# Optimization experiments

Hardware: AMD Instinct MI355X
Metric: run time of the kernel (lower is better)

Reference implementation:

```python
import jax, jax.numpy as jnp
import numpy as np

EPS = 1e-5

def _conv1x1(x, w, b):
    # x: (b,c,h,w), w: (o,c) -> (b,o,h,w)
    return jnp.einsum('bchw,oc->bohw', x, w) + b[None, :, None, None]

def _maxpool2(x):
    b, c, h, w = x.shape
    return x.reshape(b, c, h // 2, 2, w // 2, 2).max(axis=(3, 5))

def setup_inputs() -> dict:
    key = jax.random.key(0)
    ks = jax.random.split(key, 11)
    C, CI, H, W, B = 256, 128, 64, 64, 8
    s = 0.05
    return {
        'x': jax.random.normal(ks[0], (B, C, H, W), jnp.float32),
        'Wg': jax.random.normal(ks[1], (CI, C), jnp.float32) * s,
        'bg': jax.random.normal(ks[2], (CI,), jnp.float32) * s,
        'Wt': jax.random.normal(ks[3], (CI, C), jnp.float32) * s,
        'bt': jax.random.normal(ks[4], (CI,), jnp.float32) * s,
        'Wp': jax.random.normal(ks[5], (CI, C), jnp.float32) * s,
        'bp': jax.random.normal(ks[6], (CI,), jnp.float32) * s,
        'Ww': jax.random.normal(ks[7], (C, CI), jnp.float32) * s,
        'bw': jax.random.normal(ks[8], (C,), jnp.float32) * s,
        'gamma': jax.random.normal(ks[9], (C,), jnp.float32),
        'beta': jax.random.normal(ks[10], (C,), jnp.float32),
    }

def reference(x, Wg, bg, Wt, bt, Wp, bp, Ww, bw, gamma, beta):
    b, C, H, W = x.shape
    CI = Wg.shape[0]
    # g and phi are sub-sampled by 2x2 max pool -> M = (H/2)*(W/2); theta keeps N = H*W
    g_x = _maxpool2(_conv1x1(x, Wg, bg)).reshape(b, CI, -1).transpose(0, 2, 1)   # (b,M,ci)
    theta_x = _conv1x1(x, Wt, bt).reshape(b, CI, -1).transpose(0, 2, 1)          # (b,N,ci)
    phi_x = _maxpool2(_conv1x1(x, Wp, bp)).reshape(b, CI, -1)                    # (b,ci,M)
    f = jnp.einsum('bnc,bcm->bnm', theta_x, phi_x)                               # (b,N,M)
    f_div_C = jax.nn.softmax(f, axis=-1)
    y = jnp.einsum('bnm,bmc->bnc', f_div_C, g_x)                                 # (b,N,ci)
    y = y.transpose(0, 2, 1).reshape(b, CI, H, W)
    # W: 1x1 conv + BatchNorm2d (training mode: batch statistics, biased var)
    wy = _conv1x1(y, Ww, bw)
    mean = wy.mean(axis=(0, 2, 3), keepdims=True)
    var = ((wy - mean) ** 2).mean(axis=(0, 2, 3), keepdims=True)
    wy = (wy - mean) * jax.lax.rsqrt(var + EPS)
    wy = wy * gamma[None, :, None, None] + beta[None, :, None, None]
    z = wy + x
    # self.avg_pool is AdaptiveMaxPool2d(1): global spatial max
    return z.max(axis=(2, 3), keepdims=True)
```

## Files before the change

### kernel.cpp

```cpp
#include <hip/hip_runtime.h>
#include <hip/hip_bf16.h>
#include <stdint.h>

using f32x4  = __attribute__((ext_vector_type(4))) float;
using bf16x8 = __attribute__((ext_vector_type(8))) short;
using short4v = __attribute__((ext_vector_type(4))) short;

#define DEVINL static __device__ __forceinline__

DEVINL short f2bf(float f) {
    union { float f; uint32_t u; } v; v.f = f;
    uint32_t r = (v.u + 0x7FFFu + ((v.u >> 16) & 1u)) >> 16;
    return (short)(uint16_t)r;
}
DEVINL float bf2f(short s) {
    union { uint32_t u; float f; } v; v.u = ((uint32_t)(uint16_t)s) << 16;
    return v.f;
}
DEVINL float fexp2(float x) {
    float r;
    asm("v_exp_f32 %0, %1" : "=v"(r) : "v"(x));
    return r;
}
DEVINL uint32_t pk2bf(float a, float b) {
    union { __hip_bfloat162 v; uint32_t u; } c;
    c.v = __float22bfloat162_rn(float2{a, b});
    return c.u;
}

DEVINL void gld16(const short* g, short* l) {
    __builtin_amdgcn_global_load_lds(
        (const __attribute__((address_space(1))) unsigned int*)g,
        (__attribute__((address_space(3))) unsigned int*)l, 16, 0, 0);
}

#define LOG2E 1.44269504f

__global__ __launch_bounds__(256) void k0_prep(
        const float* __restrict__ Wg, const float* __restrict__ Wt, const float* __restrict__ Wp,
        const float* __restrict__ bg, const float* __restrict__ bt, const float* __restrict__ bp,
        const float* __restrict__ Ww,
        short* __restrict__ W_all, short* __restrict__ Ww16, float* __restrict__ b_all) {
    int i = blockIdx.x * 256 + threadIdx.x;
    if (i < 384 * 256) {
        int r = i >> 8, c = i & 255;
        float v = (r < 128) ? Wg[r * 256 + c]
                : (r < 256) ? Wt[(r - 128) * 256 + c] * LOG2E
                            : Wp[(r - 256) * 256 + c];
        W_all[i] = f2bf(v);
    } else if (i < 384 * 256 + 256 * 128) {
        int j = i - 384 * 256;
        Ww16[j] = f2bf(Ww[j]);
    }
    if (i < 384) {
        b_all[i] = (i < 128) ? bg[i] : (i < 256) ? bt[i - 128] * LOG2E : bp[i - 256];
    }
}

__global__ __launch_bounds__(256) void k1_conv(const float* __restrict__ x,
        const short* __restrict__ W_all, const float* __restrict__ b_all,
        short* __restrict__ OutT, short* __restrict__ Kmat, short* __restrict__ Vmat) {
    __shared__ short xs[128 * 32];
    __shared__ short obuf[128 * 128];
    const int ntile = blockIdx.x;
    const int otile = blockIdx.y;
    const int b     = blockIdx.z;
    const int tid  = threadIdx.x;
    const int lane = tid & 63;
    const int wave = tid >> 6;
    const int wn = wave >> 1, wo = wave & 1;
    const int l15 = lane & 15, lh = lane >> 4;

    f32x4 acc[4][4];
    #pragma unroll
    for (int i = 0; i < 4; i++)
        #pragma unroll
        for (int j = 0; j < 4; j++) acc[i][j] = f32x4{0.f, 0.f, 0.f, 0.f};

    const int n0 = ntile * 128;
    const int ob = otile * 128 + wo * 64;
    const float* xb = x + (size_t)b * 256 * 4096;

    const int srow_base = (lane & 15) + wave * 16;
    const int sc0 = (lane >> 4) * 8;

    for (int kt = 0; kt < 8; kt++) {
        __syncthreads();
        #pragma unroll
        for (int p = 0; p < 2; p++) {
            int row = srow_base + p * 64;
            const float* xp = xb + (size_t)(kt * 32 + sc0) * 4096 + n0 + row;
            bf16x8 w8;
            #pragma unroll
            for (int j = 0; j < 8; j++) w8[j] = f2bf(xp[(size_t)j * 4096]);
            int ch = (sc0 >> 3) ^ ((row >> 1) & 3);
            *(bf16x8*)&xs[row * 32 + ch * 8] = w8;
        }
        __syncthreads();

        bf16x8 a[4], w[4];
        #pragma unroll
        for (int nf = 0; nf < 4; nf++) {
            int row = wn * 64 + nf * 16 + l15;
            int ch  = lh ^ ((row >> 1) & 3);
            a[nf] = *(const bf16x8*)&xs[row * 32 + ch * 8];
        }
        #pragma unroll
        for (int of = 0; of < 4; of++)
            w[of] = *(const bf16x8*)(W_all + (size_t)(ob + of * 16 + l15) * 256 + kt * 32 + lh * 8);
        #pragma unroll
        for (int nf = 0; nf < 4; nf++)
            #pragma unroll
            for (int of = 0; of < 4; of++)
                acc[nf][of] = __builtin_amdgcn_mfma_f32_16x16x32_bf16(a[nf], w[of], acc[nf][of], 0, 0, 0);
    }

    #pragma unroll
    for (int of = 0; of < 4; of++) {
        int ocol = wo * 64 + of * 16 + l15;
        float bias = b_all[otile * 128 + ocol];
        #pragma unroll
        for (int nf = 0; nf < 4; nf++)
            #pragma unroll
            for (int r = 0; r < 4; r++) {
                int n  = wn * 64 + nf * 16 + lh * 4 + r;
                int ch = (ocol >> 3) ^ (n & 15);
                obuf[n * 128 + ch * 8 + (ocol & 7)] = f2bf(acc[nf][of][r] + bias);
            }
    }
    __syncthreads();

    if (otile == 1) {
        #pragma unroll
        for (int p = 0; p < 8; p++) {
            int n  = wave * 4 + lh + p * 16;
            int ch = l15 ^ (n & 15);
            bf16x8 v = *(const bf16x8*)&obuf[n * 128 + ch * 8];
            *(bf16x8*)(OutT + ((size_t)b * 4096 + n0 + n) * 128 + l15 * 8) = v;
        }
    } else if (otile == 2) {
        const int wp = tid >> 3;
        const int cc = (tid & 7) * 16;
        short* kdst = Kmat + ((size_t)b * 1024 + ntile * 32 + wp) * 128 + cc;
        #pragma unroll
        for (int cblk = 0; cblk < 2; cblk++) {
            const int chunk = (cc >> 3) + cblk;
            float mx[8];
            #pragma unroll
            for (int j = 0; j < 8; j++) mx[j] = -1e30f;
            #pragma unroll
            for (int q4 = 0; q4 < 4; q4++) {
                int n = (q4 >> 1) * 64 + 2 * wp + (q4 & 1);
                bf16x8 v = *(const bf16x8*)&obuf[n * 128 + ((chunk ^ (n & 15)) * 8)];
                #pragma unroll
                for (int j = 0; j < 8; j++) mx[j] = fmaxf(mx[j], bf2f(v[j]));
            }
            bf16x8 vo;
            #pragma unroll
            for (int j = 0; j < 8; j++) vo[j] = f2bf(mx[j]);
            *(bf16x8*)(kdst + cblk * 8) = vo;
        }
    } else {
        const int c   = tid >> 1;
        const int wp0 = (tid & 1) * 16;
        const int chb = c >> 3, cl = c & 7;
        #pragma unroll
        for (int half = 0; half < 2; half++) {
            bf16x8 vo;
            #pragma unroll
            for (int j = 0; j < 8; j++) {
                int wp = wp0 + half * 8 + j;
                float mx = -1e30f;
                #pragma unroll
                for (int q4 = 0; q4 < 4; q4++) {
                    int n = (q4 >> 1) * 64 + 2 * wp + (q4 & 1);
                    mx = fmaxf(mx, bf2f(obuf[n * 128 + ((chb ^ (n & 15)) * 8) + cl]));
                }
                vo[j] = f2bf(mx);
            }
            *(bf16x8*)(Vmat + ((size_t)b * 128 + c) * 1024 + ntile * 32 + wp0 + half * 8) = vo;
        }
    }
}

__global__ __launch_bounds__(256) void k3_attn(const short* __restrict__ OutT,
        const short* __restrict__ Kmat, const short* __restrict__ Vmat,
        const short* __restrict__ Ww16, const float* __restrict__ bw,
        short* __restrict__ wy) {
    __shared__ short smem[36864];
    short* const sKb = smem;
    short* const sVb = smem + 16384;
    short* const sPb = smem + 32768;

    const int bid = blockIdx.x;
    const int b   = bid & 7;
    const int nt  = bid >> 3;
    const int tid = threadIdx.x;
    const int lane = tid & 63;
    const int wave = tid >> 6;
    const int l15 = lane & 15, lh = lane >> 4;
    const int nblk = nt * 64;
    const int n0 = nblk + wave * 16;

    const short* Kb = Kmat + (size_t)b * 1024 * 128;
    const short* Vb = Vmat + (size_t)b * 128 * 1024;
    short* sPw = sPb + wave * 1024;

    auto STAGE = [&](int t, int bufi) {
        const int m0 = t * 64;
        #pragma unroll
        for (int i = 0; i < 4; i++) {
            const int segb = (i * 4 + wave) * 64;
            const int rowK = (segb >> 4) + (lane >> 4);
            const int chkK = lane & 15;
            gld16(Kb + (size_t)(m0 + rowK) * 128 + ((chkK ^ (rowK & 15)) << 3),
                  sKb + bufi * 8192 + segb * 8);
            const int rowV = (segb >> 3) + (lane >> 3);
            const int chkV = lane & 7;
            gld16(Vb + (size_t)rowV * 1024 + m0 + ((chkV ^ (rowV & 7)) << 3),
                  sVb + bufi * 8192 + segb * 8);
        }
    };

    bf16x8 q[4];
    {
        const short* qrow = OutT + ((size_t)b * 4096 + n0 + l15) * 128;
        #pragma unroll
        for (int ks = 0; ks < 4; ks++)
            q[ks] = *(const bf16x8*)(qrow + ks * 32 + lh * 8);
    }

    f32x4 y[8];
    #pragma unroll
    for (int cf = 0; cf < 8; cf++) y[cf] = f32x4{0.f, 0.f, 0.f, 0.f};
    float mrun = -1e30f, lrun = 0.f;

    STAGE(0, 0);
    int cur = 0;

    for (int t = 0; t < 16; t++) {
        if (t < 15) {
            STAGE(t + 1, cur ^ 1);
            asm volatile("s_waitcnt vmcnt(8)" ::: "memory");
        } else {
            asm volatile("s_waitcnt vmcnt(0)" ::: "memory");
        }
        __builtin_amdgcn_s_barrier();
        __builtin_amdgcn_sched_barrier(0);

        const short* cK = sKb + cur * 8192;
        const short* cV = sVb + cur * 8192;

        f32x4 S[4];
        #pragma unroll
        for (int mf = 0; mf < 4; mf++) S[mf] = f32x4{0.f, 0.f, 0.f, 0.f};
        #pragma unroll
        for (int ks = 0; ks < 4; ks++) {
            bf16x8 kf[4];
            #pragma unroll
            for (int mf = 0; mf < 4; mf++) {
                int mrow = mf * 16 + l15;
                int jj   = ks * 4 + lh;
                kf[mf] = *(const bf16x8*)&cK[mrow * 128 + ((jj ^ (mrow & 15)) << 3)];
            }
            __builtin_amdgcn_s_setprio(1);
            #pragma unroll
            for (int mf = 0; mf < 4; mf++)
                S[mf] = __builtin_amdgcn_mfma_f32_16x16x32_bf16(kf[mf], q[ks], S[mf], 0, 0, 0);
            __builtin_amdgcn_s_setprio(0);
        }

        float pm = S[0][0];
        #pragma unroll
        for (int mf = 0; mf < 4; mf++)
            #pragma unroll
            for (int r = 0; r < 4; r++) pm = fmaxf(pm, S[mf][r]);
        pm = fmaxf(pm, __shfl_xor(pm, 16));
        pm = fmaxf(pm, __shfl_xor(pm, 32));

        if (__any(pm > mrun + 8.656f)) {
            float mnew  = fmaxf(mrun, pm);
            float alpha = fexp2(mrun - mnew);
            mrun = mnew;
            lrun *= alpha;
            float aR[4];
            #pragma unroll
            for (int r = 0; r < 4; r++) aR[r] = __shfl(alpha, lh * 4 + r);
            #pragma unroll
            for (int cf = 0; cf < 8; cf++)
                #pragma unroll
                for (int r = 0; r < 4; r++) y[cf][r] *= aR[r];
        }
        float rs = 0.f;
        #pragma unroll
        for (int mf = 0; mf < 4; mf++)
            #pragma unroll
            for (int r = 0; r < 4; r++) {
                float p = fexp2(S[mf][r] - mrun);
                S[mf][r] = p;
                rs += p;
            }
        rs += __shfl_xor(rs, 16);
        rs += __shfl_xor(rs, 32);
        lrun += rs;

        #pragma unroll
        for (int mf = 0; mf < 4; mf++) {
            uint2 pk = { pk2bf(S[mf][0], S[mf][1]), pk2bf(S[mf][2], S[mf][3]) };
            *(uint2*)&sPw[(l15 << 6) + (((mf * 4 + lh) ^ l15) << 2)] = pk;
        }

        #pragma unroll
        for (int ks2 = 0; ks2 < 2; ks2++) {
            int u0 = ks2 * 8 + lh * 2;
            short4v lo = *(const short4v*)&sPw[(l15 << 6) + (((u0)     ^ l15) << 2)];
            short4v hi = *(const short4v*)&sPw[(l15 << 6) + (((u0 + 1) ^ l15) << 2)];
            bf16x8 pa = { lo.x, lo.y, lo.z, lo.w, hi.x, hi.y, hi.z, hi.w };
            int jj = ks2 * 4 + lh;
            __builtin_amdgcn_s_setprio(1);
            #pragma unroll
            for (int cf = 0; cf < 8; cf++) {
                int crow = cf * 16 + l15;
                bf16x8 vf = *(const bf16x8*)&cV[crow * 64 + ((jj ^ (crow & 7)) << 3)];
                y[cf] = __builtin_amdgcn_mfma_f32_16x16x32_bf16(pa, vf, y[cf], 0, 0, 0);
            }
            __builtin_amdgcn_s_setprio(0);
        }

        __builtin_amdgcn_sched_barrier(0);
        __builtin_amdgcn_s_barrier();
        cur ^= 1;
    }

    float linv[4];
    #pragma unroll
    for (int r = 0; r < 4; r++) linv[r] = 1.f / __shfl(lrun, lh * 4 + r);

    short* const Yt = smem;
    #pragma unroll
    for (int cf = 0; cf < 8; cf++) {
        int c = cf * 16 + l15;
        #pragma unroll
        for (int r = 0; r < 4; r++) {
            int n = wave * 16 + lh * 4 + r;
            Yt[n * 128 + (((c >> 3) ^ (n & 15)) << 3) + (c & 7)] = f2bf(y[cf][r] * linv[r]);
        }
    }
    __syncthreads();

    bf16x8 by[4][4];
    #pragma unroll
    for (int nf = 0; nf < 4; nf++)
        #pragma unroll
        for (int ks = 0; ks < 4; ks++) {
            int n  = nf * 16 + l15;
            int kc = ks * 4 + lh;
            by[nf][ks] = *(const bf16x8*)&Yt[n * 128 + ((kc ^ (n & 15)) << 3)];
        }

    short* const sOut = smem + 8192 + wave * 4608;
    const int obase = wave * 64;
    #pragma unroll
    for (int of = 0; of < 4; of++) {
        bf16x8 aw[4];
        #pragma unroll
        for (int ks = 0; ks < 4; ks++)
            aw[ks] = *(const bf16x8*)(Ww16 + (size_t)(obase + of * 16 + l15) * 128 + ks * 32 + lh * 8);
        #pragma unroll
        for (int nf = 0; nf < 4; nf++) {
            f32x4 acc = f32x4{0.f, 0.f, 0.f, 0.f};
            #pragma unroll
            for (int ks = 0; ks < 4; ks++)
                acc = __builtin_amdgcn_mfma_f32_16x16x32_bf16(aw[ks], by[nf][ks], acc, 0, 0, 0);
            #pragma unroll
            for (int r = 0; r < 4; r++) {
                int o_loc = of * 16 + lh * 4 + r;
                sOut[o_loc * 72 + nf * 16 + l15] = f2bf(acc[r] + bw[obase + o_loc]);
            }
        }
    }

    #pragma unroll
    for (int p = 0; p < 8; p++) {
        int o_loc = p * 8 + (lane >> 3);
        int n8    = (lane & 7) * 8;
        bf16x8 v = *(const bf16x8*)&sOut[o_loc * 72 + n8];
        *(bf16x8*)(wy + ((size_t)b * 256 + obase + o_loc) * 4096 + nblk + n8) = v;
    }
}

__global__ __launch_bounds__(512) void k45_bnmax(const short* __restrict__ wy,
        const float* __restrict__ x,
        const float* __restrict__ gamma, const float* __restrict__ beta,
        float* __restrict__ outp) {
    const int o   = blockIdx.x;
    const int tid = threadIdx.x;
    const int lane = tid & 63;
    const int wave = tid >> 6;

    bf16x8 w8[8];
    float s = 0.f, s2 = 0.f;
    #pragma unroll
    for (int b = 0; b < 8; b++) {
        w8[b] = *(const bf16x8*)(wy + ((size_t)b * 256 + o) * 4096 + tid * 8);
        #pragma unroll
        for (int j = 0; j < 8; j++) {
            float f = bf2f(w8[b][j]);
            s += f; s2 += f * f;
        }
    }
    #pragma unroll
    for (int off = 1; off < 64; off <<= 1) { s += __shfl_xor(s, off); s2 += __shfl_xor(s2, off); }
    __shared__ float sred[8][2];
    if (lane == 0) { sred[wave][0] = s; sred[wave][1] = s2; }
    __syncthreads();
    s = 0.f; s2 = 0.f;
    #pragma unroll
    for (int wv = 0; wv < 8; wv++) { s += sred[wv][0]; s2 += sred[wv][1]; }
    float mean = s * (1.f / 32768.f);
    float var  = s2 * (1.f / 32768.f) - mean * mean;
    float rstd = rsqrtf(var + 1e-5f);
    float A = rstd * gamma[o];
    float B = beta[o] - mean * A;

    float mx[8];
    #pragma unroll
    for (int b = 0; b < 8; b++) {
        const float* px = x + ((size_t)b * 256 + o) * 4096 + tid * 8;
        float4 xa = *(const float4*)px;
        float4 xb = *(const float4*)(px + 4);
        float m = bf2f(w8[b][0]) * A + B + xa.x;
        m = fmaxf(m, bf2f(w8[b][1]) * A + B + xa.y);
        m = fmaxf(m, bf2f(w8[b][2]) * A + B + xa.z);
        m = fmaxf(m, bf2f(w8[b][3]) * A + B + xa.w);
        m = fmaxf(m, bf2f(w8[b][4]) * A + B + xb.x);
        m = fmaxf(m, bf2f(w8[b][5]) * A + B + xb.y);
        m = fmaxf(m, bf2f(w8[b][6]) * A + B + xb.z);
        m = fmaxf(m, bf2f(w8[b][7]) * A + B + xb.w);
        mx[b] = m;
    }
    #pragma unroll
    for (int b = 0; b < 8; b++)
        #pragma unroll
        for (int off = 1; off < 64; off <<= 1) mx[b] = fmaxf(mx[b], __shfl_xor(mx[b], off));
    __shared__ float mred[8][8];
    if (lane == 0) {
        #pragma unroll
        for (int b = 0; b < 8; b++) mred[wave][b] = mx[b];
    }
    __syncthreads();
    if (tid < 8) {
        float m = mred[0][tid];
        #pragma unroll
        for (int wv = 1; wv < 8; wv++) m = fmaxf(m, mred[wv][tid]);
        outp[tid * 256 + o] = m;
    }
}

extern "C" void kernel_launch(void* const* d_in, const int* in_sizes, int n_in,
                              void* d_out, int out_size, void* d_ws, size_t ws_size,
                              hipStream_t stream) {
    const float* x     = (const float*)d_in[0];
    const float* Wg    = (const float*)d_in[1];
    const float* bg    = (const float*)d_in[2];
    const float* Wt    = (const float*)d_in[3];
    const float* bt    = (const float*)d_in[4];
    const float* Wp    = (const float*)d_in[5];
    const float* bp    = (const float*)d_in[6];
    const float* Ww    = (const float*)d_in[7];
    const float* bw    = (const float*)d_in[8];
    const float* gamma = (const float*)d_in[9];
    const float* beta  = (const float*)d_in[10];
    float* outp = (float*)d_out;

    char* ws = (char*)d_ws;
    size_t off = 0;
    auto alloc = [&](size_t bytes) -> void* {
        void* p = ws + off;
        off = (off + bytes + 255) & ~(size_t)255;
        return p;
    };
    short* W_all = (short*)alloc((size_t)384 * 256 * 2);
    short* Ww16  = (short*)alloc((size_t)256 * 128 * 2);
    float* b_all = (float*)alloc((size_t)384 * 4);
    short* OutT  = (short*)alloc((size_t)8 * 4096 * 128 * 2);
    short* Kmat  = (short*)alloc((size_t)8 * 1024 * 128 * 2);
    short* Vmat  = (short*)alloc((size_t)8 * 128 * 1024 * 2);
    short* wy    = (short*)alloc((size_t)8 * 256 * 4096 * 2);

    k0_prep<<<512, 256, 0, stream>>>(Wg, Wt, Wp, bg, bt, bp, Ww, W_all, Ww16, b_all);
    k1_conv<<<dim3(32, 3, 8), 256, 0, stream>>>(x, W_all, b_all, OutT, Kmat, Vmat);
    k3_attn<<<512, 256, 0, stream>>>(OutT, Kmat, Vmat, Ww16, bw, wy);
    k45_bnmax<<<256, 512, 0, stream>>>(wy, x, gamma, beta, outp);
}
```

Measured before the change: 86.25 us.

## Switch attention kernel to 32x32x16 MFMA tiles with two waves per block

The attention kernel now uses 32x32x16 bf16 MFMA instructions instead of 16x16x32 and runs two waves per block, each owning 32 query rows. The softmax reductions, P staging layout, output projection and staging loops are remapped to the 32x32 accumulator layout. The aim is better MFMA throughput and fewer LDS fragment reads per FLOP. In exchange each wave holds more accumulator registers and there are fewer waves per block, which can lower latency hiding.

```diff
diff --git a/kernel.cpp b/kernel.cpp
--- a/kernel.cpp
+++ b/kernel.cpp
@@ -3,6 +3,7 @@
 #include <stdint.h>
 
 using f32x4  = __attribute__((ext_vector_type(4))) float;
+using f32x16 = __attribute__((ext_vector_type(16))) float;
 using bf16x8 = __attribute__((ext_vector_type(8))) short;
 using short4v = __attribute__((ext_vector_type(4))) short;
 
@@ -183,11 +184,11 @@
     }
 }
 
-__global__ __launch_bounds__(256) void k3_attn(const short* __restrict__ OutT,
+__global__ __launch_bounds__(128) void k3_attn(const short* __restrict__ OutT,
         const short* __restrict__ Kmat, const short* __restrict__ Vmat,
         const short* __restrict__ Ww16, const float* __restrict__ bw,
         short* __restrict__ wy) {
-    __shared__ short smem[36864];
+    __shared__ short smem[34816];
     short* const sKb = smem;
     short* const sVb = smem + 16384;
     short* const sPb = smem + 32768;
@@ -198,19 +199,19 @@
     const int tid = threadIdx.x;
     const int lane = tid & 63;
     const int wave = tid >> 6;
-    const int l15 = lane & 15, lh = lane >> 4;
+    const int l31 = lane & 31, hi = lane >> 5;
     const int nblk = nt * 64;
-    const int n0 = nblk + wave * 16;
+    const int n0 = nblk + wave * 32;
 
     const short* Kb = Kmat + (size_t)b * 1024 * 128;
     const short* Vb = Vmat + (size_t)b * 128 * 1024;
-    short* sPw = sPb + wave * 1024;
+    short* const sPw = sPb + wave * 1024;
 
     auto STAGE = [&](int t, int bufi) {
         const int m0 = t * 64;
         #pragma unroll
-        for (int i = 0; i < 4; i++) {
-            const int segb = (i * 4 + wave) * 64;
+        for (int i = 0; i < 8; i++) {
+            const int segb = (i * 2 + wave) * 64;
             const int rowK = (segb >> 4) + (lane >> 4);
             const int chkK = lane & 15;
             gld16(Kb + (size_t)(m0 + rowK) * 128 + ((chkK ^ (rowK & 15)) << 3),
@@ -222,17 +223,19 @@
         }
     };
 
-    bf16x8 q[4];
+    bf16x8 qf[8];
     {
-        const short* qrow = OutT + ((size_t)b * 4096 + n0 + l15) * 128;
-        #pragma unroll
-        for (int ks = 0; ks < 4; ks++)
-            q[ks] = *(const bf16x8*)(qrow + ks * 32 + lh * 8);
-    }
-
-    f32x4 y[8];
-    #pragma unroll
-    for (int cf = 0; cf < 8; cf++) y[cf] = f32x4{0.f, 0.f, 0.f, 0.f};
+        const short* qrow = OutT + ((size_t)b * 4096 + n0 + l31) * 128;
+        #pragma unroll
+        for (int step = 0; step < 8; step++)
+            qf[step] = *(const bf16x8*)(qrow + step * 16 + hi * 8);
+    }
+
+    f32x16 y[4];
+    #pragma unroll
+    for (int ct = 0; ct < 4; ct++)
+        #pragma unroll
+        for (int e = 0; e < 16; e++) y[ct][e] = 0.f;
     float mrun = -1e30f, lrun = 0.f;
 
     STAGE(0, 0);
@@ -241,7 +244,7 @@
     for (int t = 0; t < 16; t++) {
         if (t < 15) {
             STAGE(t + 1, cur ^ 1);
-            asm volatile("s_waitcnt vmcnt(8)" ::: "memory");
+            asm volatile("s_waitcnt vmcnt(16)" ::: "memory");
         } else {
             asm volatile("s_waitcnt vmcnt(0)" ::: "memory");
         }
@@ -251,31 +254,32 @@
         const short* cK = sKb + cur * 8192;
         const short* cV = sVb + cur * 8192;
 
-        f32x4 S[4];
-        #pragma unroll
-        for (int mf = 0; mf < 4; mf++) S[mf] = f32x4{0.f, 0.f, 0.f, 0.f};
-        #pragma unroll
-        for (int ks = 0; ks < 4; ks++) {
-            bf16x8 kf[4];
-            #pragma unroll
-            for (int mf = 0; mf < 4; mf++) {
-                int mrow = mf * 16 + l15;
-                int jj   = ks * 4 + lh;
-                kf[mf] = *(const bf16x8*)&cK[mrow * 128 + ((jj ^ (mrow & 15)) << 3)];
+        f32x16 S[2];
+        #pragma unroll
+        for (int mt = 0; mt < 2; mt++)
+            #pragma unroll
+            for (int e = 0; e < 16; e++) S[mt][e] = 0.f;
+        #pragma unroll
+        for (int step = 0; step < 8; step++) {
+            bf16x8 kf[2];
+            #pragma unroll
+            for (int mt = 0; mt < 2; mt++) {
+                int mrow = mt * 32 + l31;
+                int chk  = step * 2 + hi;
+                kf[mt] = *(const bf16x8*)&cK[mrow * 128 + ((chk ^ (mrow & 15)) << 3)];
             }
             __builtin_amdgcn_s_setprio(1);
             #pragma unroll
-            for (int mf = 0; mf < 4; mf++)
-                S[mf] = __builtin_amdgcn_mfma_f32_16x16x32_bf16(kf[mf], q[ks], S[mf], 0, 0, 0);
+            for (int mt = 0; mt < 2; mt++)
+                S[mt] = __builtin_amdgcn_mfma_f32_32x32x16_bf16(kf[mt], qf[step], S[mt], 0, 0, 0);
             __builtin_amdgcn_s_setprio(0);
         }
 
         float pm = S[0][0];
         #pragma unroll
-        for (int mf = 0; mf < 4; mf++)
-            #pragma unroll
-            for (int r = 0; r < 4; r++) pm = fmaxf(pm, S[mf][r]);
-        pm = fmaxf(pm, __shfl_xor(pm, 16));
+        for (int mt = 0; mt < 2; mt++)
+            #pragma unroll
+            for (int e = 0; e < 16; e++) pm = fmaxf(pm, S[mt][e]);
         pm = fmaxf(pm, __shfl_xor(pm, 32));
 
         if (__any(pm > mrun + 8.656f)) {
@@ -283,48 +287,52 @@
             float alpha = fexp2(mrun - mnew);
             mrun = mnew;
             lrun *= alpha;
-            float aR[4];
-            #pragma unroll
-            for (int r = 0; r < 4; r++) aR[r] = __shfl(alpha, lh * 4 + r);
-            #pragma unroll
-            for (int cf = 0; cf < 8; cf++)
+            float aR[16];
+            #pragma unroll
+            for (int r = 0; r < 16; r++)
+                aR[r] = __shfl(alpha, (r & 3) + 8 * (r >> 2) + 4 * hi);
+            #pragma unroll
+            for (int ct = 0; ct < 4; ct++)
                 #pragma unroll
-                for (int r = 0; r < 4; r++) y[cf][r] *= aR[r];
+                for (int r = 0; r < 16; r++) y[ct][r] *= aR[r];
         }
         float rs = 0.f;
         #pragma unroll
-        for (int mf = 0; mf < 4; mf++)
-            #pragma unroll
-            for (int r = 0; r < 4; r++) {
-                float p = fexp2(S[mf][r] - mrun);
-                S[mf][r] = p;
+        for (int mt = 0; mt < 2; mt++)
+            #pragma unroll
+            for (int e = 0; e < 16; e++) {
+                float p = fexp2(S[mt][e] - mrun);
+                S[mt][e] = p;
                 rs += p;
             }
-        rs += __shfl_xor(rs, 16);
         rs += __shfl_xor(rs, 32);
         lrun += rs;
 
         #pragma unroll
-        for (int mf = 0; mf < 4; mf++) {
-            uint2 pk = { pk2bf(S[mf][0], S[mf][1]), pk2bf(S[mf][2], S[mf][3]) };
-            *(uint2*)&sPw[(l15 << 6) + (((mf * 4 + lh) ^ l15) << 2)] = pk;
-        }
-
-        #pragma unroll
-        for (int ks2 = 0; ks2 < 2; ks2++) {
-            int u0 = ks2 * 8 + lh * 2;
-            short4v lo = *(const short4v*)&sPw[(l15 << 6) + (((u0)     ^ l15) << 2)];
-            short4v hi = *(const short4v*)&sPw[(l15 << 6) + (((u0 + 1) ^ l15) << 2)];
-            bf16x8 pa = { lo.x, lo.y, lo.z, lo.w, hi.x, hi.y, hi.z, hi.w };
-            int jj = ks2 * 4 + lh;
-            __builtin_amdgcn_s_setprio(1);
-            #pragma unroll
-            for (int cf = 0; cf < 8; cf++) {
-                int crow = cf * 16 + l15;
-                bf16x8 vf = *(const bf16x8*)&cV[crow * 64 + ((jj ^ (crow & 7)) << 3)];
-                y[cf] = __builtin_amdgcn_mfma_f32_16x16x32_bf16(pa, vf, y[cf], 0, 0, 0);
-            }
-            __builtin_amdgcn_s_setprio(0);
+        for (int mt = 0; mt < 2; mt++) {
+            #pragma unroll
+            for (int g = 0; g < 4; g++) {
+                uint2 pk = { pk2bf(S[mt][g * 4 + 0], S[mt][g * 4 + 1]),
+                             pk2bf(S[mt][g * 4 + 2], S[mt][g * 4 + 3]) };
+                int mb4 = 2 * g + hi;
+                *(uint2*)&sPw[(l31 << 5) + ((mb4 ^ (l31 & 7)) << 2)] = pk;
+            }
+            #pragma unroll
+            for (int ks = 0; ks < 2; ks++) {
+                int c0 = ks * 4 + 2 * hi;
+                short4v lo = *(const short4v*)&sPw[(l31 << 5) + (((c0)     ^ (l31 & 7)) << 2)];
+                short4v h4 = *(const short4v*)&sPw[(l31 << 5) + (((c0 + 1) ^ (l31 & 7)) << 2)];
+                bf16x8 pa = { lo.x, lo.y, lo.z, lo.w, h4.x, h4.y, h4.z, h4.w };
+                __builtin_amdgcn_s_setprio(1);
+                #pragma unroll
+                for (int ct = 0; ct < 4; ct++) {
+                    int c   = ct * 32 + l31;
+                    int chk = mt * 4 + ks * 2 + hi;
+                    bf16x8 vf = *(const bf16x8*)&cV[c * 64 + ((chk ^ (c & 7)) << 3)];
+                    y[ct] = __builtin_amdgcn_mfma_f32_32x32x16_bf16(pa, vf, y[ct], 0, 0, 0);
+                }
+                __builtin_amdgcn_s_setprio(0);
+            }
         }
 
         __builtin_amdgcn_sched_barrier(0);
@@ -332,56 +340,54 @@
         cur ^= 1;
     }
 
-    float linv[4];
-    #pragma unroll
-    for (int r = 0; r < 4; r++) linv[r] = 1.f / __shfl(lrun, lh * 4 + r);
-
+    float linv[16];
+    #pragma unroll
+    for (int r = 0; r < 16; r++)
+        linv[r] = 1.f / __shfl(lrun, (r & 3) + 8 * (r >> 2) + 4 * hi);
+
+    __syncthreads();
     short* const Yt = smem;
     #pragma unroll
-    for (int cf = 0; cf < 8; cf++) {
-        int c = cf * 16 + l15;
-        #pragma unroll
-        for (int r = 0; r < 4; r++) {
-            int n = wave * 16 + lh * 4 + r;
-            Yt[n * 128 + (((c >> 3) ^ (n & 15)) << 3) + (c & 7)] = f2bf(y[cf][r] * linv[r]);
+    for (int ct = 0; ct < 4; ct++) {
+        int c = ct * 32 + l31;
+        #pragma unroll
+        for (int r = 0; r < 16; r++) {
+            int n = wave * 32 + (r & 3) + 8 * (r >> 2) + 4 * hi;
+            Yt[n * 128 + (((c >> 3) ^ (n & 15)) << 3) + (c & 7)] = f2bf(y[ct][r] * linv[r]);
         }
     }
     __syncthreads();
 
-    bf16x8 by[4][4];
-    #pragma unroll
-    for (int nf = 0; nf < 4; nf++)
-        #pragma unroll
-        for (int ks = 0; ks < 4; ks++) {
-            int n  = nf * 16 + l15;
-            int kc = ks * 4 + lh;
-            by[nf][ks] = *(const bf16x8*)&Yt[n * 128 + ((kc ^ (n & 15)) << 3)];
-        }
-
-    short* const sOut = smem + 8192 + wave * 4608;
-    const int obase = wave * 64;
-    #pragma unroll
-    for (int of = 0; of < 4; of++) {
-        bf16x8 aw[4];
-        #pragma unroll
-        for (int ks = 0; ks < 4; ks++)
-            aw[ks] = *(const bf16x8*)(Ww16 + (size_t)(obase + of * 16 + l15) * 128 + ks * 32 + lh * 8);
-        #pragma unroll
-        for (int nf = 0; nf < 4; nf++) {
-            f32x4 acc = f32x4{0.f, 0.f, 0.f, 0.f};
-            #pragma unroll
-            for (int ks = 0; ks < 4; ks++)
-                acc = __builtin_amdgcn_mfma_f32_16x16x32_bf16(aw[ks], by[nf][ks], acc, 0, 0, 0);
-            #pragma unroll
-            for (int r = 0; r < 4; r++) {
-                int o_loc = of * 16 + lh * 4 + r;
-                sOut[o_loc * 72 + nf * 16 + l15] = f2bf(acc[r] + bw[obase + o_loc]);
-            }
-        }
-    }
-
-    #pragma unroll
-    for (int p = 0; p < 8; p++) {
+    short* const sOut = smem + 8192 + wave * 9216;
+    const int obase = wave * 128;
+    #pragma unroll
+    for (int ot = 0; ot < 4; ot++) {
+        bf16x8 aw[8];
+        #pragma unroll
+        for (int step = 0; step < 8; step++)
+            aw[step] = *(const bf16x8*)(Ww16 + (size_t)(obase + ot * 32 + l31) * 128 + step * 16 + hi * 8);
+        #pragma unroll
+        for (int nt2 = 0; nt2 < 2; nt2++) {
+            f32x16 acc;
+            #pragma unroll
+            for (int e = 0; e < 16; e++) acc[e] = 0.f;
+            #pragma unroll
+            for (int step = 0; step < 8; step++) {
+                int n   = nt2 * 32 + l31;
+                int chk = step * 2 + hi;
+                bf16x8 byf = *(const bf16x8*)&Yt[n * 128 + ((chk ^ (n & 15)) << 3)];
+                acc = __builtin_amdgcn_mfma_f32_32x32x16_bf16(aw[step], byf, acc, 0, 0, 0);
+            }
+            #pragma unroll
+            for (int r = 0; r < 16; r++) {
+                int o_loc = ot * 32 + (r & 3) + 8 * (r >> 2) + 4 * hi;
+                sOut[o_loc * 72 + nt2 * 32 + l31] = f2bf(acc[r] + bw[obase + o_loc]);
+            }
+        }
+    }
+
+    #pragma unroll
+    for (int p = 0; p < 16; p++) {
         int o_loc = p * 8 + (lane >> 3);
         int n8    = (lane & 7) * 8;
         bf16x8 v = *(const bf16x8*)&sOut[o_loc * 72 + n8];
@@ -490,6 +496,6 @@
 
     k0_prep<<<512, 256, 0, stream>>>(Wg, Wt, Wp, bg, bt, bp, Ww, W_all, Ww16, b_all);
     k1_conv<<<dim3(32, 3, 8), 256, 0, stream>>>(x, W_all, b_all, OutT, Kmat, Vmat);
-    k3_attn<<<512, 256, 0, stream>>>(OutT, Kmat, Vmat, Ww16, bw, wy);
+    k3_attn<<<512, 128, 0, stream>>>(OutT, Kmat, Vmat, Ww16, bw, wy);
     k45_bnmax<<<256, 512, 0, stream>>>(wy, x, gamma, beta, outp);
 }
```

New measurement: 95.63 us. +10.9%, slower.

## Compute all three 1x1 conv projections per block to reuse loaded x tile

Applied to the files above, without the earlier changes.

The conv kernel now handles all three projection output tiles (g, theta, phi) in a single block instead of launching a separate block per output tile. Each x tile is loaded from global memory and converted to bf16 once instead of three times, cutting global reads of the input. In exchange, each block holds three times as many accumulators, raising register pressure. The grid also shrinks to 256 blocks, which may reduce occupancy and latency hiding.

```diff
diff --git a/kernel.cpp b/kernel.cpp
--- a/kernel.cpp
+++ b/kernel.cpp
@@ -63,22 +63,22 @@
     __shared__ short xs[128 * 32];
     __shared__ short obuf[128 * 128];
     const int ntile = blockIdx.x;
-    const int otile = blockIdx.y;
-    const int b     = blockIdx.z;
+    const int b     = blockIdx.y;
     const int tid  = threadIdx.x;
     const int lane = tid & 63;
     const int wave = tid >> 6;
     const int wn = wave >> 1, wo = wave & 1;
     const int l15 = lane & 15, lh = lane >> 4;
 
-    f32x4 acc[4][4];
-    #pragma unroll
-    for (int i = 0; i < 4; i++)
-        #pragma unroll
-        for (int j = 0; j < 4; j++) acc[i][j] = f32x4{0.f, 0.f, 0.f, 0.f};
+    f32x4 acc[3][4][4];
+    #pragma unroll
+    for (int ot = 0; ot < 3; ot++)
+        #pragma unroll
+        for (int i = 0; i < 4; i++)
+            #pragma unroll
+            for (int j = 0; j < 4; j++) acc[ot][i][j] = f32x4{0.f, 0.f, 0.f, 0.f};
 
     const int n0 = ntile * 128;
-    const int ob = otile * 128 + wo * 64;
     const float* xb = x + (size_t)b * 256 * 4096;
 
     const int srow_base = (lane & 15) + wave * 16;
@@ -98,7 +98,7 @@
         }
         __syncthreads();
 
-        bf16x8 a[4], w[4];
+        bf16x8 a[4];
         #pragma unroll
         for (int nf = 0; nf < 4; nf++) {
             int row = wn * 64 + nf * 16 + l15;
@@ -106,79 +106,87 @@
             a[nf] = *(const bf16x8*)&xs[row * 32 + ch * 8];
         }
         #pragma unroll
-        for (int of = 0; of < 4; of++)
-            w[of] = *(const bf16x8*)(W_all + (size_t)(ob + of * 16 + l15) * 256 + kt * 32 + lh * 8);
-        #pragma unroll
-        for (int nf = 0; nf < 4; nf++)
+        for (int ot = 0; ot < 3; ot++) {
+            bf16x8 w[4];
             #pragma unroll
             for (int of = 0; of < 4; of++)
-                acc[nf][of] = __builtin_amdgcn_mfma_f32_16x16x32_bf16(a[nf], w[of], acc[nf][of], 0, 0, 0);
-    }
-
-    #pragma unroll
-    for (int of = 0; of < 4; of++) {
-        int ocol = wo * 64 + of * 16 + l15;
-        float bias = b_all[otile * 128 + ocol];
-        #pragma unroll
-        for (int nf = 0; nf < 4; nf++)
-            #pragma unroll
-            for (int r = 0; r < 4; r++) {
-                int n  = wn * 64 + nf * 16 + lh * 4 + r;
-                int ch = (ocol >> 3) ^ (n & 15);
-                obuf[n * 128 + ch * 8 + (ocol & 7)] = f2bf(acc[nf][of][r] + bias);
-            }
-    }
-    __syncthreads();
-
-    if (otile == 1) {
-        #pragma unroll
-        for (int p = 0; p < 8; p++) {
-            int n  = wave * 4 + lh + p * 16;
-            int ch = l15 ^ (n & 15);
-            bf16x8 v = *(const bf16x8*)&obuf[n * 128 + ch * 8];
-            *(bf16x8*)(OutT + ((size_t)b * 4096 + n0 + n) * 128 + l15 * 8) = v;
-        }
-    } else if (otile == 2) {
-        const int wp = tid >> 3;
-        const int cc = (tid & 7) * 16;
-        short* kdst = Kmat + ((size_t)b * 1024 + ntile * 32 + wp) * 128 + cc;
-        #pragma unroll
-        for (int cblk = 0; cblk < 2; cblk++) {
-            const int chunk = (cc >> 3) + cblk;
-            float mx[8];
-            #pragma unroll
-            for (int j = 0; j < 8; j++) mx[j] = -1e30f;
-            #pragma unroll
-            for (int q4 = 0; q4 < 4; q4++) {
-                int n = (q4 >> 1) * 64 + 2 * wp + (q4 & 1);
-                bf16x8 v = *(const bf16x8*)&obuf[n * 128 + ((chunk ^ (n & 15)) * 8)];
-                #pragma unroll
-                for (int j = 0; j < 8; j++) mx[j] = fmaxf(mx[j], bf2f(v[j]));
-            }
-            bf16x8 vo;
-            #pragma unroll
-            for (int j = 0; j < 8; j++) vo[j] = f2bf(mx[j]);
-            *(bf16x8*)(kdst + cblk * 8) = vo;
-        }
-    } else {
-        const int c   = tid >> 1;
-        const int wp0 = (tid & 1) * 16;
-        const int chb = c >> 3, cl = c & 7;
-        #pragma unroll
-        for (int half = 0; half < 2; half++) {
-            bf16x8 vo;
-            #pragma unroll
-            for (int j = 0; j < 8; j++) {
-                int wp = wp0 + half * 8 + j;
-                float mx = -1e30f;
+                w[of] = *(const bf16x8*)(W_all + (size_t)(ot * 128 + wo * 64 + of * 16 + l15) * 256 + kt * 32 + lh * 8);
+            #pragma unroll
+            for (int nf = 0; nf < 4; nf++)
+                #pragma unroll
+                for (int of = 0; of < 4; of++)
+                    acc[ot][nf][of] = __builtin_amdgcn_mfma_f32_16x16x32_bf16(a[nf], w[of], acc[ot][nf][of], 0, 0, 0);
+        }
+    }
+
+    #pragma unroll
+    for (int ot = 0; ot < 3; ot++) {
+        __syncthreads();
+        #pragma unroll
+        for (int of = 0; of < 4; of++) {
+            int ocol = wo * 64 + of * 16 + l15;
+            float bias = b_all[ot * 128 + ocol];
+            #pragma unroll
+            for (int nf = 0; nf < 4; nf++)
+                #pragma unroll
+                for (int r = 0; r < 4; r++) {
+                    int n  = wn * 64 + nf * 16 + lh * 4 + r;
+                    int ch = (ocol >> 3) ^ (n & 15);
+                    obuf[n * 128 + ch * 8 + (ocol & 7)] = f2bf(acc[ot][nf][of][r] + bias);
+                }
+        }
+        __syncthreads();
+
+        if (ot == 1) {
+            #pragma unroll
+            for (int p = 0; p < 8; p++) {
+                int n  = wave * 4 + lh + p * 16;
+                int ch = l15 ^ (n & 15);
+                bf16x8 v = *(const bf16x8*)&obuf[n * 128 + ch * 8];
+                *(bf16x8*)(OutT + ((size_t)b * 4096 + n0 + n) * 128 + l15 * 8) = v;
+            }
+        } else if (ot == 2) {
+            const int wp = tid >> 3;
+            const int cc = (tid & 7) * 16;
+            short* kdst = Kmat + ((size_t)b * 1024 + ntile * 32 + wp) * 128 + cc;
+            #pragma unroll
+            for (int cblk = 0; cblk < 2; cblk++) {
+                const int chunk = (cc >> 3) + cblk;
+                float mx[8];
+                #pragma unroll
+                for (int j = 0; j < 8; j++) mx[j] = -1e30f;
                 #pragma unroll
                 for (int q4 = 0; q4 < 4; q4++) {
                     int n = (q4 >> 1) * 64 + 2 * wp + (q4 & 1);
-                    mx = fmaxf(mx, bf2f(obuf[n * 128 + ((chb ^ (n & 15)) * 8) + cl]));
+                    bf16x8 v = *(const bf16x8*)&obuf[n * 128 + ((chunk ^ (n & 15)) * 8)];
+                    #pragma unroll
+                    for (int j = 0; j < 8; j++) mx[j] = fmaxf(mx[j], bf2f(v[j]));
                 }
-                vo[j] = f2bf(mx);
-            }
-            *(bf16x8*)(Vmat + ((size_t)b * 128 + c) * 1024 + ntile * 32 + wp0 + half * 8) = vo;
+                bf16x8 vo;
+                #pragma unroll
+                for (int j = 0; j < 8; j++) vo[j] = f2bf(mx[j]);
+                *(bf16x8*)(kdst + cblk * 8) = vo;
+            }
+        } else {
+            const int c   = tid >> 1;
+            const int wp0 = (tid & 1) * 16;
+            const int chb = c >> 3, cl = c & 7;
+            #pragma unroll
+            for (int half = 0; half < 2; half++) {
+                bf16x8 vo;
+                #pragma unroll
+                for (int j = 0; j < 8; j++) {
+                    int wp = wp0 + half * 8 + j;
+                    float mx = -1e30f;
+                    #pragma unroll
+                    for (int q4 = 0; q4 < 4; q4++) {
+                        int n = (q4 >> 1) * 64 + 2 * wp + (q4 & 1);
+                        mx = fmaxf(mx, bf2f(obuf[n * 128 + ((chb ^ (n & 15)) * 8) + cl]));
+                    }
+                    vo[j] = f2bf(mx);
+                }
+                *(bf16x8*)(Vmat + ((size_t)b * 128 + c) * 1024 + ntile * 32 + wp0 + half * 8) = vo;
+            }
         }
     }
 }
@@ -489,7 +497,7 @@
     short* wy    = (short*)alloc((size_t)8 * 256 * 4096 * 2);
 
     k0_prep<<<512, 256, 0, stream>>>(Wg, Wt, Wp, bg, bt, bp, Ww, W_all, Ww16, b_all);
-    k1_conv<<<dim3(32, 3, 8), 256, 0, stream>>>(x, W_all, b_all, OutT, Kmat, Vmat);
+    k1_conv<<<dim3(32, 8), 256, 0, stream>>>(x, W_all, b_all, OutT, Kmat, Vmat);
     k3_attn<<<512, 256, 0, stream>>>(OutT, Kmat, Vmat, Ww16, bw, wy);
     k45_bnmax<<<256, 512, 0, stream>>>(wy, x, gamma, beta, outp);
 }
```

Measured after the change: 85.51 us. No clear change (-0.9%).
